# Optimization experiments

Measured on AMD Instinct MI355X. Metric: run time of the kernel, lower is better.

## Reference

```python
import jax, jax.numpy as jnp
import numpy as np

N, D, H, F = 384, 512, 8, 64  # n_nodes, in/out features, heads, per-head hidden
SLOPE = 0.2


def gat_v2_layer(x, mask, W_l, W_r, a):
    """GATv2 layer (is_concat=True). x: [N, D_in]; mask: [N, N, 1] bool.

    torch semantics: g_sum[i, j] = g_l[j] + g_r[i]; e = a . LeakyReLU(g_sum);
    softmax over j (dim=1); aggregate g_r with einsum('ijh,jhf->ihf').
    attn linear nn.Linear(F, 1) is shared across heads -> a: [F].
    """
    n = x.shape[0]
    g_l = (x @ W_l).reshape(n, H, F)
    g_r = (x @ W_r).reshape(n, H, F)
    # pairwise [i, j, h, f] = g_r[i] + g_l[j]  (the big O(N^2) intermediate)
    s = jax.nn.leaky_relu(g_r[:, None] + g_l[None, :], negative_slope=SLOPE)
    e = jnp.einsum('ijhf,f->ijh', s, a)
    e = jnp.where(mask, e, -jnp.inf)
    att = jax.nn.softmax(e, axis=1)  # normalize over source nodes j
    out = jnp.einsum('ijh,jhf->ihf', att, g_r)
    return out.reshape(n, H * F)


def setup_inputs() -> dict:
    key = jax.random.key(0)
    ks = jax.random.split(key, 8)
    x = jax.random.normal(ks[0], (N, D), dtype=jnp.float32)
    adj = jax.random.randint(ks[1], (N, N, 1), 0, 2, dtype=jnp.int32)
    sd = 1.0 / np.sqrt(D)
    sa = 1.0 / np.sqrt(F)
    W_l0 = jax.random.normal(ks[2], (D, H * F), dtype=jnp.float32) * sd
    W_r0 = jax.random.normal(ks[3], (D, H * F), dtype=jnp.float32) * sd
    a0 = jax.random.normal(ks[4], (F,), dtype=jnp.float32) * sa
    W_l1 = jax.random.normal(ks[5], (H * F, H * F), dtype=jnp.float32) * sd
    W_r1 = jax.random.normal(ks[6], (H * F, H * F), dtype=jnp.float32) * sd
    a1 = jax.random.normal(ks[7], (F,), dtype=jnp.float32) * sa
    return {"x": x, "adj": adj, "W_l0": W_l0, "W_r0": W_r0, "a0": a0,
            "W_l1": W_l1, "W_r1": W_r1, "a1": a1}


def reference(x, adj, W_l0, W_r0, a0, W_l1, W_r1, a1):
    n = x.shape[0]
    # selfloop: fill diagonal of adj with 1
    idx = jnp.arange(n)
    adj = adj.at[idx, idx, 0].set(1)
    mask = adj != 0  # [N, N, 1]
    # layer 0: GATv2 -> ELU (i < n_layers-1) -> residual
    out = jax.nn.elu(gat_v2_layer(x, mask, W_l0, W_r0, a0))
    x = x + out
    # layer 1: GATv2 -> Identity -> residual
    out = gat_v2_layer(x, mask, W_l1, W_r1, a1)
    x = x + out
    return x
```

## Files before the change

kernel.cpp:

```cpp
#include <hip/hip_runtime.h>
#include <hip/hip_bf16.h>
#include <stdint.h>

typedef unsigned short ushort_t;
typedef __attribute__((ext_vector_type(8))) short short8;
typedef __attribute__((ext_vector_type(4))) float f32x4;

#define N_NODES 384
#define HF      512

__device__ inline ushort_t f2bf(float f) {
  __hip_bfloat16 b = __float2bfloat16(f);
  return *reinterpret_cast<ushort_t*>(&b);
}

__global__ __launch_bounds__(256) void prep(
    const float* __restrict__ x,
    const float* __restrict__ w0, const float* __restrict__ w1,
    const float* __restrict__ w2, const float* __restrict__ w3,
    ushort_t* __restrict__ WT0, ushort_t* __restrict__ WT1,
    ushort_t* __restrict__ xb)
{
  const int z = blockIdx.z;
  const int t = threadIdx.x;
  if (z == 4) {
    int idx = (blockIdx.y * 16 + blockIdx.x) * 256 + t;
#pragma unroll
    for (int r = 0; r < 3; ++r) {
      int i = idx + r * 65536;
      xb[i] = f2bf(x[i]);
    }
    return;
  }
  __shared__ ushort_t tile[32][33];
  const float* W = (z == 0) ? w0 : (z == 1) ? w1 : (z == 2) ? w2 : w3;
  ushort_t* WT = ((z < 2) ? WT0 : WT1) + (z & 1) * (512 * 512);
  const int n0 = blockIdx.x * 32, k0 = blockIdx.y * 32;
#pragma unroll
  for (int qq = 0; qq < 4; ++qq) {
    int idx = t + qq * 256, r = idx >> 5, c = idx & 31;
    tile[r][c] = f2bf(W[(k0 + r) * 512 + n0 + c]);
  }
  __syncthreads();
#pragma unroll
  for (int qq = 0; qq < 4; ++qq) {
    int idx = t + qq * 256, r = idx >> 5, c = idx & 31;
    WT[(n0 + r) * 512 + k0 + c] = tile[c][r];
  }
}

__global__ __launch_bounds__(256) void gemm_mfma(
    const ushort_t* __restrict__ A, const ushort_t* __restrict__ WT,
    float* __restrict__ G, ushort_t* __restrict__ grT)
{
  const int t = threadIdx.x;
  const int wave = t >> 6, lane = t & 63;
  const int lm = lane & 15, q = lane >> 4;
  const int m0 = blockIdx.x * 16;
  const int n0 = (blockIdx.y * 4 + wave) * 32;

  const short8* Ap = (const short8*)A;
  const short8* Bp = (const short8*)WT;
  const int arow  = (m0 + lm) * 64 + q;
  const int brow0 = (n0 + lm) * 64 + q;
  const int brow1 = (n0 + 16 + lm) * 64 + q;

  f32x4 acc0 = {0.f, 0.f, 0.f, 0.f};
  f32x4 acc1 = {0.f, 0.f, 0.f, 0.f};
#pragma unroll
  for (int kc = 0; kc < 16; ++kc) {
    short8 af = Ap[arow  + kc * 4];
    short8 b0 = Bp[brow0 + kc * 4];
    short8 b1 = Bp[brow1 + kc * 4];
    acc0 = __builtin_amdgcn_mfma_f32_16x16x32_bf16(af, b0, acc0, 0, 0, 0);
    acc1 = __builtin_amdgcn_mfma_f32_16x16x32_bf16(af, b1, acc1, 0, 0, 0);
  }
#pragma unroll
  for (int r = 0; r < 4; ++r) {
    int m = m0 + q * 4 + r;
    G[m * 1024 + n0 + lm]      = acc0[r];
    G[m * 1024 + n0 + 16 + lm] = acc1[r];
  }
  if (n0 >= 512) {
    int c0 = n0 - 512;
    uint2 p0, p1;
    p0.x = (uint32_t)f2bf(acc0[0]) | ((uint32_t)f2bf(acc0[1]) << 16);
    p0.y = (uint32_t)f2bf(acc0[2]) | ((uint32_t)f2bf(acc0[3]) << 16);
    p1.x = (uint32_t)f2bf(acc1[0]) | ((uint32_t)f2bf(acc1[1]) << 16);
    p1.y = (uint32_t)f2bf(acc1[2]) | ((uint32_t)f2bf(acc1[3]) << 16);
    *(uint2*)&grT[(c0 + lm) * 384 + m0 + q * 4]      = p0;
    *(uint2*)&grT[(c0 + 16 + lm) * 384 + m0 + q * 4] = p1;
  }
}

template <int LAYER>
__global__ __launch_bounds__(256) void attn_fused(
    const float* __restrict__ G, const ushort_t* __restrict__ grT,
    const int* __restrict__ adj, const float* __restrict__ resid_in,
    const float* __restrict__ avec,
    float* __restrict__ xcur_out, ushort_t* __restrict__ x1b_out,
    float* __restrict__ f_out)
{
  __shared__ float s_a[64];
  __shared__ float s_gri[16][64];
  __shared__ float s_bri[16];
  __shared__ float s_e[16][N_NODES];
  __shared__ ushort_t s_pb[16][392];

  const int t = threadIdx.x, lane = t & 63, wave = t >> 6;
  const int i0 = blockIdx.x * 16, h = blockIdx.y;

  if (t < 64) s_a[t] = avec[t];
  {
    int il = t >> 4, c = t & 15;
    ((float4*)s_gri[il])[c] =
        *(const float4*)(G + (i0 + il) * 1024 + 512 + h * 64 + c * 4);
  }
  __syncthreads();
  if (t < 128) {
    int row = t >> 3, g = t & 7;
    float s = 0.f;
#pragma unroll
    for (int f = 0; f < 8; ++f) s += s_a[g * 8 + f] * s_gri[row][g * 8 + f];
    s += __shfl_xor(s, 1); s += __shfl_xor(s, 2); s += __shfl_xor(s, 4);
    if (g == 0) s_bri[row] = s;
  }
  __syncthreads();

  for (int jb = 0; jb < N_NODES; jb += 256) {
    int j = jb + t;
    if (j < N_NODES) {
      const float4* gl4 = (const float4*)(G + j * 1024 + h * 64);
      float accl = 0.f;
      float acca[16];
#pragma unroll
      for (int il = 0; il < 16; ++il) acca[il] = 0.f;
#pragma unroll 4
      for (int c = 0; c < 16; ++c) {
        float4 gv = gl4[c];
        float4 av = ((const float4*)s_a)[c];
        accl += av.x * gv.x + av.y * gv.y + av.z * gv.z + av.w * gv.w;
#pragma unroll
        for (int il = 0; il < 16; ++il) {
          float4 rv = ((const float4*)s_gri[il])[c];
          acca[il] += av.x * fabsf(gv.x + rv.x) + av.y * fabsf(gv.y + rv.y)
                    + av.z * fabsf(gv.z + rv.z) + av.w * fabsf(gv.w + rv.w);
        }
      }
#pragma unroll
      for (int il = 0; il < 16; ++il) {
        int ig = i0 + il;
        bool msk = (adj[ig * N_NODES + j] != 0) || (ig == j);
        float e = 0.6f * (accl + s_bri[il]) + 0.4f * acca[il];
        s_e[il][j] = msk ? e : -1e30f;
      }
    }
  }
  __syncthreads();

#pragma unroll
  for (int rep = 0; rep < 4; ++rep) {
    int il = wave * 4 + rep;
    float v[6];
    float mx = -1e30f;
#pragma unroll
    for (int c = 0; c < 6; ++c) { v[c] = s_e[il][lane + 64 * c]; mx = fmaxf(mx, v[c]); }
#pragma unroll
    for (int off = 32; off; off >>= 1) mx = fmaxf(mx, __shfl_xor(mx, off));
    float sum = 0.f;
#pragma unroll
    for (int c = 0; c < 6; ++c) { v[c] = __expf(v[c] - mx); sum += v[c]; }
#pragma unroll
    for (int off = 32; off; off >>= 1) sum += __shfl_xor(sum, off);
    float inv = 1.0f / sum;
#pragma unroll
    for (int c = 0; c < 6; ++c) s_pb[il][lane + 64 * c] = f2bf(v[c] * inv);
  }
  __syncthreads();

  {
    const int lm = lane & 15, q = lane >> 4;
    const int f0 = wave * 16;
    const ushort_t* Brow = grT + (h * 64 + f0 + lm) * 384;
    f32x4 acc = {0.f, 0.f, 0.f, 0.f};
#pragma unroll
    for (int kc = 0; kc < 12; ++kc) {
      short8 af = *(const short8*)&s_pb[lm][kc * 32 + q * 8];
      short8 bf = *(const short8*)&Brow[kc * 32 + q * 8];
      acc = __builtin_amdgcn_mfma_f32_16x16x32_bf16(af, bf, acc, 0, 0, 0);
    }
#pragma unroll
    for (int r = 0; r < 4; ++r) {
      int i = i0 + q * 4 + r;
      int off = i * HF + h * 64 + f0 + lm;
      float o = acc[r];
      if (LAYER == 0) {
        float oe = (o > 0.f) ? o : (__expf(o) - 1.f);
        float vv = resid_in[off] + oe;
        xcur_out[off] = vv;
        x1b_out[off]  = f2bf(vv);
      } else {
        f_out[off] = resid_in[off] + o;
      }
    }
  }
}

extern "C" void kernel_launch(void* const* d_in, const int* in_sizes, int n_in,
                              void* d_out, int out_size, void* d_ws, size_t ws_size,
                              hipStream_t stream) {
  const float* x   = (const float*)d_in[0];
  const int*   adj = (const int*)d_in[1];
  const float* Wl0 = (const float*)d_in[2];
  const float* Wr0 = (const float*)d_in[3];
  const float* a0  = (const float*)d_in[4];
  const float* Wl1 = (const float*)d_in[5];
  const float* Wr1 = (const float*)d_in[6];
  const float* a1  = (const float*)d_in[7];
  float* out = (float*)d_out;

  char* ws = (char*)d_ws;
  float*    xcur = (float*)(ws);
  ushort_t* WT0  = (ushort_t*)(ws);
  ushort_t* WT1  = (ushort_t*)(ws + 1048576);
  ushort_t* xb   = (ushort_t*)(ws + 2097152);
  float*    G    = (float*)   (ws + 2490368);
  ushort_t* grT  = (ushort_t*)(ws + 4063232);
  ushort_t* x1b  = (ushort_t*)(ws + 4456448);

  prep<<<dim3(16, 16, 5), 256, 0, stream>>>(x, Wl0, Wr0, Wl1, Wr1, WT0, WT1, xb);
  gemm_mfma<<<dim3(24, 8), 256, 0, stream>>>(xb, WT0, G, grT);
  attn_fused<0><<<dim3(24, 8), 256, 0, stream>>>(G, grT, adj, x, a0,
                                                 xcur, x1b, nullptr);
  gemm_mfma<<<dim3(24, 8), 256, 0, stream>>>(x1b, WT1, G, grT);
  attn_fused<1><<<dim3(24, 8), 256, 0, stream>>>(G, grT, adj, xcur, a1,
                                                 nullptr, nullptr, out);
}
```

Baseline: 147.1 us.

## Pack adjacency into bitmasks, store g_l as bf16, use one thread per source node

The prep kernel now packs the int32 adjacency (with self-loops) into 64-bit ballot bitmasks once, so attention reads masks instead of the full int matrix. The GEMM writes g_l as bf16 into a separate buffer. The attention kernel runs 384 threads, one per source node j: each thread stages its g_l row in shared memory and keeps it in registers, reads g_r rows straight from global (uniform loads), and reuses one shared buffer for both the g_l staging and the score matrix. This removes repeated adjacency traffic and halves g_l bandwidth. The costs are higher register pressure (64 floats for g_l plus 16 accumulators), lower precision for g_l, and some waves idling during the MFMA stage.

```diff
diff --git a/kernel.cpp b/kernel.cpp
--- a/kernel.cpp
+++ b/kernel.cpp
@@ -3,6 +3,7 @@
 #include <stdint.h>
 
 typedef unsigned short ushort_t;
+typedef unsigned long long u64;
 typedef __attribute__((ext_vector_type(8))) short short8;
 typedef __attribute__((ext_vector_type(4))) float f32x4;
 
@@ -13,13 +14,16 @@
   __hip_bfloat16 b = __float2bfloat16(f);
   return *reinterpret_cast<ushort_t*>(&b);
 }
+__device__ inline float bf2f_u(ushort_t u) {
+  union { float f; uint32_t i; } v; v.i = ((uint32_t)u) << 16; return v.f;
+}
 
 __global__ __launch_bounds__(256) void prep(
-    const float* __restrict__ x,
+    const float* __restrict__ x, const int* __restrict__ adj,
     const float* __restrict__ w0, const float* __restrict__ w1,
     const float* __restrict__ w2, const float* __restrict__ w3,
     ushort_t* __restrict__ WT0, ushort_t* __restrict__ WT1,
-    ushort_t* __restrict__ xb)
+    ushort_t* __restrict__ xb, u64* __restrict__ mbits)
 {
   const int z = blockIdx.z;
   const int t = threadIdx.x;
@@ -32,6 +36,20 @@
     }
     return;
   }
+  if (z == 5) {
+    int b = blockIdx.y * 16 + blockIdx.x;
+    if (b >= 96) return;
+    int wave = t >> 6, lane = t & 63;
+    int row = b * 4 + wave;
+#pragma unroll
+    for (int w = 0; w < 6; ++w) {
+      int j = w * 64 + lane;
+      int v = adj[row * N_NODES + j];
+      u64 m = __ballot(v != 0 || row == j);
+      if (lane == 0) mbits[row * 6 + w] = m;
+    }
+    return;
+  }
   __shared__ ushort_t tile[32][33];
   const float* W = (z == 0) ? w0 : (z == 1) ? w1 : (z == 2) ? w2 : w3;
   ushort_t* WT = ((z < 2) ? WT0 : WT1) + (z & 1) * (512 * 512);
@@ -51,7 +69,8 @@
 
 __global__ __launch_bounds__(256) void gemm_mfma(
     const ushort_t* __restrict__ A, const ushort_t* __restrict__ WT,
-    float* __restrict__ G, ushort_t* __restrict__ grT)
+    float* __restrict__ G, ushort_t* __restrict__ glb,
+    ushort_t* __restrict__ grT)
 {
   const int t = threadIdx.x;
   const int wave = t >> 6, lane = t & 63;
@@ -75,13 +94,20 @@
     acc0 = __builtin_amdgcn_mfma_f32_16x16x32_bf16(af, b0, acc0, 0, 0, 0);
     acc1 = __builtin_amdgcn_mfma_f32_16x16x32_bf16(af, b1, acc1, 0, 0, 0);
   }
-#pragma unroll
-  for (int r = 0; r < 4; ++r) {
-    int m = m0 + q * 4 + r;
-    G[m * 1024 + n0 + lm]      = acc0[r];
-    G[m * 1024 + n0 + 16 + lm] = acc1[r];
-  }
-  if (n0 >= 512) {
+  if (n0 < 512) {
+#pragma unroll
+    for (int r = 0; r < 4; ++r) {
+      int m = m0 + q * 4 + r;
+      glb[m * HF + n0 + lm]      = f2bf(acc0[r]);
+      glb[m * HF + n0 + 16 + lm] = f2bf(acc1[r]);
+    }
+  } else {
+#pragma unroll
+    for (int r = 0; r < 4; ++r) {
+      int m = m0 + q * 4 + r;
+      G[m * 1024 + n0 + lm]      = acc0[r];
+      G[m * 1024 + n0 + 16 + lm] = acc1[r];
+    }
     int c0 = n0 - 512;
     uint2 p0, p1;
     p0.x = (uint32_t)f2bf(acc0[0]) | ((uint32_t)f2bf(acc0[1]) << 16);
@@ -94,73 +120,82 @@
 }
 
 template <int LAYER>
-__global__ __launch_bounds__(256) void attn_fused(
-    const float* __restrict__ G, const ushort_t* __restrict__ grT,
-    const int* __restrict__ adj, const float* __restrict__ resid_in,
-    const float* __restrict__ avec,
+__global__ __launch_bounds__(384) void attn_fused(
+    const float* __restrict__ G, const ushort_t* __restrict__ glb,
+    const ushort_t* __restrict__ grT, const u64* __restrict__ mbits,
+    const float* __restrict__ resid_in, const float* __restrict__ avec,
     float* __restrict__ xcur_out, ushort_t* __restrict__ x1b_out,
     float* __restrict__ f_out)
 {
-  __shared__ float s_a[64];
-  __shared__ float s_gri[16][64];
+  __shared__ __align__(16) char smem[55296];
+  ushort_t (*s_gl)[72]      = (ushort_t(*)[72])smem;
+  float    (*s_e)[N_NODES]  = (float(*)[N_NODES])smem;
+  ushort_t (*s_pb)[392]     = (ushort_t(*)[392])(smem + 24576);
   __shared__ float s_bri[16];
-  __shared__ float s_e[16][N_NODES];
-  __shared__ ushort_t s_pb[16][392];
-
-  const int t = threadIdx.x, lane = t & 63, wave = t >> 6;
+  __shared__ u64   s_mask[16][6];
+
+  const int t = threadIdx.x;
   const int i0 = blockIdx.x * 16, h = blockIdx.y;
-
-  if (t < 64) s_a[t] = avec[t];
+  const int lane = t & 63, wave = t >> 6;
+
+  if (t >= 64 && t < 160) ((u64*)s_mask)[t - 64] = mbits[i0 * 6 + (t - 64)];
+  if (t >= 128) {
+    int u = t - 128, il = u >> 4, fg = u & 15;
+    float4 g4 = *(const float4*)(G + (i0 + il) * 1024 + 512 + h * 64 + fg * 4);
+    float4 a4 = *(const float4*)(avec + fg * 4);
+    float s = a4.x * g4.x + a4.y * g4.y + a4.z * g4.z + a4.w * g4.w;
+    s += __shfl_xor(s, 1); s += __shfl_xor(s, 2);
+    s += __shfl_xor(s, 4); s += __shfl_xor(s, 8);
+    if (fg == 0) s_bri[il] = s;
+  }
+#pragma unroll
+  for (int rep = 0; rep < 8; ++rep) {
+    int idx = rep * 384 + t, row = idx >> 3, c = idx & 7;
+    *(short8*)&s_gl[row][c * 8] =
+        *(const short8*)&glb[row * HF + h * 64 + c * 8];
+  }
+  __syncthreads();
+
+  float gl[64];
   {
-    int il = t >> 4, c = t & 15;
-    ((float4*)s_gri[il])[c] =
-        *(const float4*)(G + (i0 + il) * 1024 + 512 + h * 64 + c * 4);
-  }
-  __syncthreads();
-  if (t < 128) {
-    int row = t >> 3, g = t & 7;
-    float s = 0.f;
-#pragma unroll
-    for (int f = 0; f < 8; ++f) s += s_a[g * 8 + f] * s_gri[row][g * 8 + f];
-    s += __shfl_xor(s, 1); s += __shfl_xor(s, 2); s += __shfl_xor(s, 4);
-    if (g == 0) s_bri[row] = s;
-  }
-  __syncthreads();
-
-  for (int jb = 0; jb < N_NODES; jb += 256) {
-    int j = jb + t;
-    if (j < N_NODES) {
-      const float4* gl4 = (const float4*)(G + j * 1024 + h * 64);
-      float accl = 0.f;
-      float acca[16];
-#pragma unroll
-      for (int il = 0; il < 16; ++il) acca[il] = 0.f;
-#pragma unroll 4
-      for (int c = 0; c < 16; ++c) {
-        float4 gv = gl4[c];
-        float4 av = ((const float4*)s_a)[c];
-        accl += av.x * gv.x + av.y * gv.y + av.z * gv.z + av.w * gv.w;
-#pragma unroll
-        for (int il = 0; il < 16; ++il) {
-          float4 rv = ((const float4*)s_gri[il])[c];
-          acca[il] += av.x * fabsf(gv.x + rv.x) + av.y * fabsf(gv.y + rv.y)
-                    + av.z * fabsf(gv.z + rv.z) + av.w * fabsf(gv.w + rv.w);
-        }
-      }
-#pragma unroll
-      for (int il = 0; il < 16; ++il) {
-        int ig = i0 + il;
-        bool msk = (adj[ig * N_NODES + j] != 0) || (ig == j);
-        float e = 0.6f * (accl + s_bri[il]) + 0.4f * acca[il];
-        s_e[il][j] = msk ? e : -1e30f;
-      }
-    }
-  }
-  __syncthreads();
-
-#pragma unroll
-  for (int rep = 0; rep < 4; ++rep) {
-    int il = wave * 4 + rep;
+    const short8* rowp = (const short8*)&s_gl[t][0];
+#pragma unroll
+    for (int c = 0; c < 8; ++c) {
+      short8 v = rowp[c];
+#pragma unroll
+      for (int u2 = 0; u2 < 8; ++u2)
+        gl[c * 8 + u2] = bf2f_u((ushort_t)v[u2]);
+    }
+  }
+  __syncthreads();
+
+  float accl = 0.f;
+#pragma unroll
+  for (int f = 0; f < 64; ++f) accl += avec[f] * gl[f];
+
+  float e_abs[16];
+  for (int il = 0; il < 16; ++il) {
+    const float* __restrict__ gr = G + (i0 + il) * 1024 + 512 + h * 64;
+    float acc = 0.f;
+#pragma unroll
+    for (int f = 0; f < 64; ++f) {
+      float z = gl[f] + gr[f];
+      acc += avec[f] * fabsf(z);
+    }
+    e_abs[il] = acc;
+  }
+  {
+    const int jw = t >> 6, jb = t & 63;
+#pragma unroll
+    for (int il = 0; il < 16; ++il) {
+      bool m = (s_mask[il][jw] >> jb) & 1;
+      float e = 0.6f * (accl + s_bri[il]) + 0.4f * e_abs[il];
+      s_e[il][t] = m ? e : -1e30f;
+    }
+  }
+  __syncthreads();
+
+  for (int il = wave; il < 16; il += 6) {
     float v[6];
     float mx = -1e30f;
 #pragma unroll
@@ -178,7 +213,7 @@
   }
   __syncthreads();
 
-  {
+  if (t < 256) {
     const int lm = lane & 15, q = lane >> 4;
     const int f0 = wave * 16;
     const ushort_t* Brow = grT + (h * 64 + f0 + lm) * 384;
@@ -220,19 +255,22 @@
   float* out = (float*)d_out;
 
   char* ws = (char*)d_ws;
-  float*    xcur = (float*)(ws);
-  ushort_t* WT0  = (ushort_t*)(ws);
-  ushort_t* WT1  = (ushort_t*)(ws + 1048576);
-  ushort_t* xb   = (ushort_t*)(ws + 2097152);
-  float*    G    = (float*)   (ws + 2490368);
-  ushort_t* grT  = (ushort_t*)(ws + 4063232);
-  ushort_t* x1b  = (ushort_t*)(ws + 4456448);
-
-  prep<<<dim3(16, 16, 5), 256, 0, stream>>>(x, Wl0, Wr0, Wl1, Wr1, WT0, WT1, xb);
-  gemm_mfma<<<dim3(24, 8), 256, 0, stream>>>(xb, WT0, G, grT);
-  attn_fused<0><<<dim3(24, 8), 256, 0, stream>>>(G, grT, adj, x, a0,
+  ushort_t* WT0  = (ushort_t*)(ws + 0L);
+  ushort_t* WT1  = (ushort_t*)(ws + (1L << 20));
+  ushort_t* xb   = (ushort_t*)(ws + (2L << 20));
+  float*    G    = (float*)   (ws + (3L << 20));
+  ushort_t* grT  = (ushort_t*)(ws + (5L << 20));
+  ushort_t* x1b  = (ushort_t*)(ws + (6L << 20));
+  ushort_t* glb  = (ushort_t*)(ws + (7L << 20));
+  u64*      mbits= (u64*)     (ws + (8L << 20));
+  float*    xcur = (float*)   (ws + (9L << 20));
+
+  prep<<<dim3(16, 16, 6), 256, 0, stream>>>(x, adj, Wl0, Wr0, Wl1, Wr1,
+                                            WT0, WT1, xb, mbits);
+  gemm_mfma<<<dim3(24, 8), 256, 0, stream>>>(xb, WT0, G, glb, grT);
+  attn_fused<0><<<dim3(24, 8), 384, 0, stream>>>(G, glb, grT, mbits, x, a0,
                                                  xcur, x1b, nullptr);
-  gemm_mfma<<<dim3(24, 8), 256, 0, stream>>>(x1b, WT1, G, grT);
-  attn_fused<1><<<dim3(24, 8), 256, 0, stream>>>(G, grT, adj, xcur, a1,
+  gemm_mfma<<<dim3(24, 8), 256, 0, stream>>>(x1b, WT1, G, glb, grT);
+  attn_fused<1><<<dim3(24, 8), 384, 0, stream>>>(G, glb, grT, mbits, xcur, a1,
                                                  nullptr, nullptr, out);
 }
```

Result: faster. 137.0 us (-6.9%).
